# Optimization experiments

Measured on AMD Instinct MI355X. Metric: run time of the kernel, lower is better.

## Reference

```python
import jax, jax.numpy as jnp
import numpy as np

HEAD_NUM = 4
B, S, D = 8, 1024, 512


def setup_inputs() -> dict:
    k = jax.random.key(0)
    kq, kk, kv = jax.random.split(k, 3)
    return {
        "query": jax.random.normal(kq, (B, S, D), dtype=jnp.float32),
        "key": jax.random.normal(kk, (B, S, D), dtype=jnp.float32),
        "value": jax.random.normal(kv, (B, S, D), dtype=jnp.float32),
    }


def _corr_attention(q, k, v):
    # q,k,v: [B, H, S, hd]
    score = jnp.einsum('bhqd,bhkd->bhqk', q, k)  # raw dot products
    len_q = jnp.sqrt(jnp.sum(q * q, axis=-1))    # [B,H,S]
    len_k = jnp.sqrt(jnp.sum(k * k, axis=-1))    # [B,H,S]
    score = score / (len_q[..., :, None] * len_k[..., None, :])  # cosine similarity
    signal = jnp.sign(score)
    flat = jnp.abs(score).reshape(-1)            # global flatten across B,H,S,S
    n = flat.shape[0]
    idx = jnp.argsort(-flat)                     # descending sort indices
    prob = (jnp.arange(n, dtype=flat.dtype) + 1.0) / n  # (1/n, 2/n, ..., 1)
    ranked = flat.at[idx].set(prob)              # rank-transform: largest -> smallest prob
    score = (-jnp.log(ranked)).reshape(signal.shape) * signal
    return jnp.einsum('bhqk,bhkd->bhqd', score, v)


def reference(query, key, value):
    b, s, d = query.shape
    h = HEAD_NUM
    q = query.reshape(b, s, h, -1).transpose(0, 2, 1, 3)
    k = key.reshape(b, s, h, -1).transpose(0, 2, 1, 3)
    v = value.reshape(b, s, h, -1).transpose(0, 2, 1, 3)
    out = _corr_attention(q, k, v)               # [B,H,S,hd]
    return out.transpose(0, 2, 1, 3).reshape(b, s, d)
```

## Files before the change

kernel.cpp:

```cpp
#include <hip/hip_runtime.h>
#include <math.h>

#define BB 8
#define SS 1024
#define DD 512
#define HH 4
#define HD 128
#define N_SC (BB*HH*SS*SS)

#define NB 8192
#define BINS 13107.2f
#define NBLK 2048
#define NP2 32

#define OFF_S     0
#define SZ_S      ((size_t)N_SC*2)
#define OFF_QN    (OFF_S + SZ_S)
#define SZ_QN     ((size_t)BB*SS*DD*2)
#define OFF_KN    (OFF_QN + SZ_QN)
#define OFF_VT    (OFF_KN + SZ_QN)
#define OFF_PARTS (OFF_VT + SZ_QN)
#define SZ_PARTS  ((size_t)NBLK*(NB/4)*4)
#define OFF_WMAG  (OFF_PARTS + SZ_PARTS)
#define OFF_PART2 (OFF_WMAG + (size_t)NB*2)

typedef __bf16 bf16x8 __attribute__((ext_vector_type(8)));
typedef float  f32x4  __attribute__((ext_vector_type(4)));
typedef unsigned short ushort_t;

__device__ __forceinline__ unsigned bf16rne(float x) {
  unsigned b = __float_as_uint(x);
  return (b + 0x7FFFu + ((b >> 16) & 1u)) >> 16;
}
__device__ __forceinline__ unsigned sbin(float s) {
  return (unsigned)fminf(fabsf(s)*BINS, 8191.0f);
}

__global__ __launch_bounds__(256) void prep_vt_kernel(
    const float* __restrict__ q, const float* __restrict__ k,
    const float* __restrict__ v,
    unsigned* __restrict__ qn, unsigned* __restrict__ kn,
    unsigned* __restrict__ vt) {
  __shared__ float T[64][65];
  int t = threadIdx.x;
  if (blockIdx.x < 16384) {
    int lane = t & 63;
    int row = blockIdx.x*4 + (t >> 6);
    const float* src; unsigned* dst; int r;
    if (row < 32768) { src = q; dst = qn; r = row; }
    else             { src = k; dst = kn; r = row - 32768; }
    int b = r >> 12, s = (r >> 2) & 1023, h = r & 3;
    float2 vv = *(const float2*)(src + ((size_t)(b*1024 + s))*512 + h*128 + lane*2);
    float sum = vv.x*vv.x + vv.y*vv.y;
    #pragma unroll
    for (int off = 32; off; off >>= 1) sum += __shfl_xor(sum, off, 64);
    float inv = rsqrtf(sum);
    unsigned u = bf16rne(vv.x*inv) | (bf16rne(vv.y*inv) << 16);
    dst[(size_t)((b*4 + h)*1024 + s)*64 + lane] = u;
  } else {
    int vb = blockIdx.x - 16384;
    int s0 = (vb & 15)*64, d0 = ((vb >> 4) & 1)*64, bh = vb >> 5;
    int b = bh >> 2, h = bh & 3;
    #pragma unroll
    for (int i = 0; i < 16; i++) {
      int idx = t + i*256, rs = idx >> 6, cd = idx & 63;
      T[rs][cd] = v[((size_t)(b*1024 + s0 + rs))*512 + h*128 + d0 + cd];
    }
    __syncthreads();
    #pragma unroll
    for (int i = 0; i < 8; i++) {
      int idx = t + i*256, rd = idx >> 5, c2 = (idx & 31)*2;
      unsigned u = bf16rne(T[c2][rd]) | (bf16rne(T[c2+1][rd]) << 16);
      vt[(size_t)(bh*128 + d0 + rd)*512 + (s0 + c2)/2] = u;
    }
  }
}

__global__ __launch_bounds__(256) void scores_hist_kernel(
    const ushort_t* __restrict__ qn, const ushort_t* __restrict__ kn,
    ushort_t* __restrict__ S, unsigned* __restrict__ parts) {
  __shared__ ushort_t Qs[128*128];
  __shared__ ushort_t Ks[128*128];
  __shared__ unsigned h8[NB/4];
  int t = threadIdx.x;
  int L = blockIdx.x;
  int bh = L & 31, tile = L >> 5;
  int sq0 = (tile >> 3)*128, sk0 = (tile & 7)*128;

  #pragma unroll
  for (int i = 0; i < 8; i++) h8[t + i*256] = 0;

  const uint4* qg = (const uint4*)qn + (size_t)(bh*1024 + sq0)*16;
  const uint4* kg = (const uint4*)kn + (size_t)(bh*1024 + sk0)*16;
  #pragma unroll
  for (int i = 0; i < 8; i++) {
    int idx = t + i*256, row = idx >> 4, g = idx & 15;
    int sw = g ^ (row & 15);
    *(uint4*)&Qs[row*128 + sw*8] = qg[row*16 + g];
    *(uint4*)&Ks[row*128 + sw*8] = kg[row*16 + g];
  }
  __syncthreads();

  int w = t >> 6, lane = t & 63, m16 = lane & 15, q2 = lane >> 4;
  int wm = (w >> 1)*64, wn = (w & 1)*64;
  f32x4 acc[4][4];
  #pragma unroll
  for (int i = 0; i < 4; i++)
    #pragma unroll
    for (int j = 0; j < 4; j++) acc[i][j] = (f32x4){0.f,0.f,0.f,0.f};

  #pragma unroll
  for (int ks = 0; ks < 4; ks++) {
    int sw = ((ks*4 + q2) ^ m16)*8;
    bf16x8 a[4], bb[4];
    #pragma unroll
    for (int i = 0; i < 4; i++) a[i]  = *(const bf16x8*)&Qs[(wm + i*16 + m16)*128 + sw];
    #pragma unroll
    for (int j = 0; j < 4; j++) bb[j] = *(const bf16x8*)&Ks[(wn + j*16 + m16)*128 + sw];
    #pragma unroll
    for (int i = 0; i < 4; i++)
      #pragma unroll
      for (int j = 0; j < 4; j++)
        acc[i][j] = __builtin_amdgcn_mfma_f32_16x16x32_bf16(a[i], bb[j], acc[i][j], 0, 0, 0);
  }

  size_t Sbase = (size_t)bh << 20;
  #pragma unroll
  for (int i = 0; i < 4; i++)
    #pragma unroll
    for (int p = 0; p < 4; p++) {
      int row = sq0 + wm + i*16 + q2*4 + p;
      #pragma unroll
      for (int j = 0; j < 4; j++) {
        int col = sk0 + wn + j*16 + m16;
        unsigned u = bf16rne(acc[i][j][p]);
        S[Sbase + ((size_t)row << 10) + col] = (ushort_t)u;
        unsigned bin = sbin(__uint_as_float(u << 16));
        atomicAdd(&h8[bin >> 2], 1u << ((bin & 3)*8));
      }
    }
  __syncthreads();

  unsigned* dst = parts + (size_t)L*(NB/4);
  #pragma unroll
  for (int i = 0; i < 8; i++) dst[t + i*256] = h8[t + i*256];
}

__global__ __launch_bounds__(256) void reduce1_kernel(
    const unsigned* __restrict__ parts, unsigned* __restrict__ parts2) {
  int g = blockIdx.x*256 + threadIdx.x;
  int p0 = blockIdx.y*64;
  unsigned s0 = 0, s1 = 0, s2 = 0, s3 = 0;
  #pragma unroll 8
  for (int p = p0; p < p0 + 64; p++) {
    unsigned w = parts[(size_t)p*(NB/4) + g];
    s0 += w & 0xFFu; s1 += (w >> 8) & 0xFFu;
    s2 += (w >> 16) & 0xFFu; s3 += w >> 24;
  }
  uint4 o = {s0, s1, s2, s3};
  ((uint4*)parts2)[(size_t)blockIdx.y*(NB/4) + g] = o;
}

__global__ __launch_bounds__(1024) void scan_kernel(
    const unsigned* __restrict__ parts2, ushort_t* __restrict__ wmag) {
  __shared__ unsigned d[1024];
  int t = threadIdx.x;
  unsigned loc[8] = {0,0,0,0,0,0,0,0};
  #pragma unroll 4
  for (int p = 0; p < NP2; p++) {
    uint4 a = ((const uint4*)parts2)[(size_t)p*(NB/4) + t*2];
    uint4 b2 = ((const uint4*)parts2)[(size_t)p*(NB/4) + t*2 + 1];
    loc[0] += a.x;  loc[1] += a.y;  loc[2] += a.z;  loc[3] += a.w;
    loc[4] += b2.x; loc[5] += b2.y; loc[6] += b2.z; loc[7] += b2.w;
  }
  unsigned tot = 0;
  #pragma unroll
  for (int j = 0; j < 8; j++) tot += loc[j];
  d[t] = tot; __syncthreads();
  for (int off = 1; off < 1024; off <<= 1) {
    unsigned x = (t >= off) ? d[t - off] : 0u;
    __syncthreads();
    d[t] += x;
    __syncthreads();
  }
  unsigned run = d[t] - tot;
  const float inv_n = 1.0f / (float)N_SC;
  #pragma unroll
  for (int j = 0; j < 8; j++) {
    run += loc[j];
    float rm = (float)(N_SC - run) + 0.5f*(float)(loc[j] + 1u);
    wmag[t*8 + j] = (ushort_t)bf16rne(-logf(rm * inv_n));
  }
}

__global__ __launch_bounds__(512) void out_kernel(
    const ushort_t* __restrict__ S, const ushort_t* __restrict__ wmag,
    const ushort_t* __restrict__ vt, float* __restrict__ out) {
  __shared__ ushort_t Vs[2][128*128];
  __shared__ ushort_t Wl[NB];
  int t = threadIdx.x;
  int L = blockIdx.x;
  int bh = L & 31, q0 = (L >> 5)*64;
  int b = bh >> 2, h = bh & 3;

  #pragma unroll
  for (int i = 0; i < 2; i++)
    ((uint4*)Wl)[t + i*512] = ((const uint4*)wmag)[t + i*512];

  int w = t >> 6, lane = t & 63, m16 = lane & 15, q2 = lane >> 4;
  int qt = w & 3, kh = w >> 2;
  int qw = q0 + qt*16;
  int half = t >> 8, tl = t & 255;
  const ushort_t* Srow = S + ((size_t)(bh*1024 + qw + m16) << 10);
  const uint4* vg = (const uint4*)vt + (size_t)bh*128*128;

  f32x4 oacc[8];
  #pragma unroll
  for (int j = 0; j < 8; j++) oacc[j] = (f32x4){0.f,0.f,0.f,0.f};

  for (int kc4 = 0; kc4 < 4; kc4++) {
    int kcs = half*4 + kc4;
    #pragma unroll
    for (int i = 0; i < 8; i++) {
      int idx = tl + i*256, row = idx >> 4, g = idx & 15;
      *(uint4*)&Vs[half][row*128 + (g ^ (row & 15))*8] = vg[row*128 + kcs*16 + g];
    }
    __syncthreads();

    int kc = kh*4 + kc4;
    #pragma unroll
    for (int ks = 0; ks < 4; ks++) {
      uint4 sv = *(const uint4*)&Srow[kc*128 + ks*32 + q2*8];
      unsigned sc[4] = {sv.x, sv.y, sv.z, sv.w};
      union { bf16x8 v; unsigned u[4]; } af;
      #pragma unroll
      for (int m = 0; m < 4; m++) {
        float flo = __uint_as_float(sc[m] << 16);
        float fhi = __uint_as_float(sc[m] & 0xFFFF0000u);
        unsigned wlo = (flo == 0.f) ? 0u
                       : (unsigned)Wl[sbin(flo)] | ((flo < 0.f) ? 0x8000u : 0u);
        unsigned whi = (fhi == 0.f) ? 0u
                       : (unsigned)Wl[sbin(fhi)] | ((fhi < 0.f) ? 0x8000u : 0u);
        af.u[m] = wlo | (whi << 16);
      }
      int sw = ((ks*4 + q2) ^ m16)*8;
      #pragma unroll
      for (int j = 0; j < 8; j++) {
        bf16x8 bb = *(const bf16x8*)&Vs[kh][(j*16 + m16)*128 + sw];
        oacc[j] = __builtin_amdgcn_mfma_f32_16x16x32_bf16(af.v, bb, oacc[j], 0, 0, 0);
      }
    }
    __syncthreads();
  }

  float* R = (float*)Vs;
  if (kh == 1) {
    #pragma unroll
    for (int j = 0; j < 8; j++)
      #pragma unroll
      for (int p = 0; p < 4; p++)
        R[qt*(16*129) + (q2*4 + p)*129 + j*16 + m16] = oacc[j][p];
  }
  __syncthreads();
  if (kh == 0) {
    #pragma unroll
    for (int j = 0; j < 8; j++)
      #pragma unroll
      for (int p = 0; p < 4; p++)
        oacc[j][p] += R[qt*(16*129) + (q2*4 + p)*129 + j*16 + m16];
    #pragma unroll
    for (int p = 0; p < 4; p++) {
      int qrow = qw + q2*4 + p;
      #pragma unroll
      for (int j = 0; j < 8; j++)
        out[(size_t)(b*1024 + qrow)*512 + h*128 + j*16 + m16] = oacc[j][p];
    }
  }
}

extern "C" void kernel_launch(void* const* d_in, const int* in_sizes, int n_in,
                              void* d_out, int out_size, void* d_ws, size_t ws_size,
                              hipStream_t stream) {
  const float* q = (const float*)d_in[0];
  const float* k = (const float*)d_in[1];
  const float* v = (const float*)d_in[2];
  float* out = (float*)d_out;
  char* ws = (char*)d_ws;

  ushort_t* Sbuf  = (ushort_t*)(ws + OFF_S);
  unsigned* qn    = (unsigned*)(ws + OFF_QN);
  unsigned* kn    = (unsigned*)(ws + OFF_KN);
  unsigned* vtb   = (unsigned*)(ws + OFF_VT);
  unsigned* parts = (unsigned*)(ws + OFF_PARTS);
  ushort_t* wmag  = (ushort_t*)(ws + OFF_WMAG);
  unsigned* part2 = (unsigned*)(ws + OFF_PART2);

  hipLaunchKernelGGL(prep_vt_kernel, dim3(17408), dim3(256), 0, stream, q, k, v, qn, kn, vtb);
  hipLaunchKernelGGL(scores_hist_kernel, dim3(NBLK), dim3(256), 0, stream,
                     (const ushort_t*)qn, (const ushort_t*)kn, Sbuf, parts);
  hipLaunchKernelGGL(reduce1_kernel, dim3(8, NP2), dim3(256), 0, stream, parts, part2);
  hipLaunchKernelGGL(scan_kernel, dim3(1), dim3(1024), 0, stream, part2, wmag);
  hipLaunchKernelGGL(out_kernel, dim3(512), dim3(512), 0, stream,
                     (const ushort_t*)Sbuf, wmag, (const ushort_t*)vtb, out);
}
```

Before: 167.3 us.

## Stage score tiles through LDS with coalesced loads in output kernel

The output kernel now loads each 64x128 chunk of the bf16 score matrix cooperatively into a swizzled shared-memory tile, instead of having each lane read score rows straight from global memory. The K split between the two wave halves moves inside each 128-wide chunk, so both halves share one V tile per iteration rather than each keeping its own half. The aim is to coalesce the score reads and cut the per-iteration V footprint. In exchange the loop runs eight barriered iterations instead of four, with smaller loads per iteration and less memory-level parallelism per step.

Result: no change. 166.3 us (-0.6%).

```diff
diff --git a/kernel.cpp b/kernel.cpp
--- a/kernel.cpp
+++ b/kernel.cpp
@@ -196,8 +196,10 @@
 __global__ __launch_bounds__(512) void out_kernel(
     const ushort_t* __restrict__ S, const ushort_t* __restrict__ wmag,
     const ushort_t* __restrict__ vt, float* __restrict__ out) {
-  __shared__ ushort_t Vs[2][128*128];
+  __shared__ ushort_t Buf[128*128 + 64*128];
   __shared__ ushort_t Wl[NB];
+  ushort_t* Vs = Buf;
+  ushort_t* Ss = Buf + 128*128;
   int t = threadIdx.x;
   int L = blockIdx.x;
   int bh = L & 31, q0 = (L >> 5)*64;
@@ -210,29 +212,32 @@
   int w = t >> 6, lane = t & 63, m16 = lane & 15, q2 = lane >> 4;
   int qt = w & 3, kh = w >> 2;
   int qw = q0 + qt*16;
-  int half = t >> 8, tl = t & 255;
-  const ushort_t* Srow = S + ((size_t)(bh*1024 + qw + m16) << 10);
   const uint4* vg = (const uint4*)vt + (size_t)bh*128*128;
+  const uint4* sg = (const uint4*)S + (size_t)bh*1024*128;
 
   f32x4 oacc[8];
   #pragma unroll
   for (int j = 0; j < 8; j++) oacc[j] = (f32x4){0.f,0.f,0.f,0.f};
 
-  for (int kc4 = 0; kc4 < 4; kc4++) {
-    int kcs = half*4 + kc4;
-    #pragma unroll
-    for (int i = 0; i < 8; i++) {
-      int idx = tl + i*256, row = idx >> 4, g = idx & 15;
-      *(uint4*)&Vs[half][row*128 + (g ^ (row & 15))*8] = vg[row*128 + kcs*16 + g];
-    }
-    __syncthreads();
-
-    int kc = kh*4 + kc4;
-    #pragma unroll
-    for (int ks = 0; ks < 4; ks++) {
-      uint4 sv = *(const uint4*)&Srow[kc*128 + ks*32 + q2*8];
+  for (int kc = 0; kc < 8; kc++) {
+    #pragma unroll
+    for (int i = 0; i < 4; i++) {
+      int idx = t + i*512, row = idx >> 4, g = idx & 15;
+      *(uint4*)&Vs[row*128 + (g ^ (row & 15))*8] = vg[row*128 + kc*16 + g];
+    }
+    #pragma unroll
+    for (int i = 0; i < 2; i++) {
+      int idx = t + i*512, row = idx >> 4, g = idx & 15;
+      *(uint4*)&Ss[row*128 + (g ^ (row & 15))*8] = sg[(size_t)(q0 + row)*128 + kc*16 + g];
+    }
+    __syncthreads();
+
+    #pragma unroll
+    for (int u = 0; u < 2; u++) {
+      int gk = kh*8 + u*4 + q2;
+      uint4 sv = *(const uint4*)&Ss[(qt*16 + m16)*128 + (gk ^ m16)*8];
       unsigned sc[4] = {sv.x, sv.y, sv.z, sv.w};
-      union { bf16x8 v; unsigned u[4]; } af;
+      union { bf16x8 v; unsigned u2[4]; } af;
       #pragma unroll
       for (int m = 0; m < 4; m++) {
         float flo = __uint_as_float(sc[m] << 16);
@@ -241,25 +246,24 @@
                        : (unsigned)Wl[sbin(flo)] | ((flo < 0.f) ? 0x8000u : 0u);
         unsigned whi = (fhi == 0.f) ? 0u
                        : (unsigned)Wl[sbin(fhi)] | ((fhi < 0.f) ? 0x8000u : 0u);
-        af.u[m] = wlo | (whi << 16);
+        af.u2[m] = wlo | (whi << 16);
       }
-      int sw = ((ks*4 + q2) ^ m16)*8;
       #pragma unroll
       for (int j = 0; j < 8; j++) {
-        bf16x8 bb = *(const bf16x8*)&Vs[kh][(j*16 + m16)*128 + sw];
+        bf16x8 bb = *(const bf16x8*)&Vs[(j*16 + m16)*128 + (gk ^ m16)*8];
         oacc[j] = __builtin_amdgcn_mfma_f32_16x16x32_bf16(af.v, bb, oacc[j], 0, 0, 0);
       }
     }
     __syncthreads();
   }
 
-  float* R = (float*)Vs;
+  float* R = (float*)Buf;
   if (kh == 1) {
     #pragma unroll
     for (int j = 0; j < 8; j++)
       #pragma unroll
       for (int p = 0; p < 4; p++)
-        R[qt*(16*129) + (q2*4 + p)*129 + j*16 + m16] = oacc[j][p];
+        R[(qt*16 + q2*4 + p)*129 + j*16 + m16] = oacc[j][p];
   }
   __syncthreads();
   if (kh == 0) {
@@ -267,7 +271,7 @@
     for (int j = 0; j < 8; j++)
       #pragma unroll
       for (int p = 0; p < 4; p++)
-        oacc[j][p] += R[qt*(16*129) + (q2*4 + p)*129 + j*16 + m16];
+        oacc[j][p] += R[(qt*16 + q2*4 + p)*129 + j*16 + m16];
     #pragma unroll
     for (int p = 0; p < 4; p++) {
       int qrow = qw + q2*4 + p;
```
